# Kernel tuning notes

Measured on AMD Instinct MI355X. Metric: run time of the kernel, lower is better.

## Reference

```python
import jax, jax.numpy as jnp
import numpy as np

N, E = 50000, 800000
HID, HEADS, EDIM = 64, 4, 3
NEG_SLOPE = 0.2
LN_EPS = 1e-5


def setup_inputs() -> dict:
    key = jax.random.key(0)
    ks = jax.random.split(key, 12)
    h = jax.random.normal(ks[0], (N, HID), dtype=jnp.float32)
    edge_index = jax.random.randint(ks[1], (2, E), 0, N, dtype=jnp.int64)
    edge_attr = jax.random.normal(ks[2], (E, EDIM), dtype=jnp.float32)
    t = jax.random.uniform(ks[3], (1,), dtype=jnp.float32)
    s = 1.0 / np.sqrt(HID)
    W = jax.random.normal(ks[4], (HID, HEADS * HID), dtype=jnp.float32) * s
    att_src = jax.random.normal(ks[5], (1, HEADS, HID), dtype=jnp.float32) * s
    att_dst = jax.random.normal(ks[6], (1, HEADS, HID), dtype=jnp.float32) * s
    W_edge = jax.random.normal(ks[7], (EDIM, HEADS * HID), dtype=jnp.float32) * s
    att_edge = jax.random.normal(ks[8], (1, HEADS, HID), dtype=jnp.float32) * s
    bias = jnp.zeros((HID,), dtype=jnp.float32)
    ln_gamma = jnp.ones((HID,), dtype=jnp.float32)
    ln_beta = jnp.zeros((HID,), dtype=jnp.float32)
    return {"t": t, "h": h, "edge_index": edge_index, "edge_attr": edge_attr,
            "W": W, "att_src": att_src, "att_dst": att_dst, "W_edge": W_edge,
            "att_edge": att_edge, "bias": bias, "ln_gamma": ln_gamma, "ln_beta": ln_beta}


def reference(t, h, edge_index, edge_attr, W, att_src, att_dst, W_edge, att_edge, bias, ln_gamma, ln_beta):
    # GATConv (PyG, edge_dim>0, add_self_loops=False, concat=False, eval mode)
    x = (h @ W).reshape(N, HEADS, HID)                     # [N,H,C]
    a_src = (x * att_src).sum(-1)                          # [N,H]
    a_dst = (x * att_dst).sum(-1)                          # [N,H]
    e = (edge_attr @ W_edge).reshape(E, HEADS, HID)        # [E,H,C]
    a_edge = (e * att_edge).sum(-1)                        # [E,H]
    src, dst = edge_index[0], edge_index[1]
    alpha = a_src[src] + a_dst[dst] + a_edge               # [E,H]
    alpha = jax.nn.leaky_relu(alpha, NEG_SLOPE)
    # softmax over edges sharing the same destination node
    amax = jax.ops.segment_max(alpha, dst, num_segments=N)  # [N,H]
    ex = jnp.exp(alpha - amax[dst])
    esum = jax.ops.segment_sum(ex, dst, num_segments=N)     # [N,H]
    alpha = ex / (esum[dst] + 1e-16)
    msg = x[src] * alpha[:, :, None]                        # [E,H,C]
    out = jax.ops.segment_sum(msg, dst, num_segments=N)     # [N,H,C]
    out = out.mean(axis=1) + bias                           # concat=False -> head mean
    # LayerNorm + SiLU
    mu = out.mean(-1, keepdims=True)
    var = ((out - mu) ** 2).mean(-1, keepdims=True)
    y = (out - mu) * jax.lax.rsqrt(var + LN_EPS) * ln_gamma + ln_beta
    return y * jax.nn.sigmoid(y)
```

## Files before the change

kernel.cpp:

```cpp
#include <hip/hip_runtime.h>
#include <hip/hip_bf16.h>

#define HIDC 64
#define NEG_SLOPE 0.2f
#define SCAN_G 128

typedef __hip_bfloat16 bf16;
typedef short bf16x8 __attribute__((ext_vector_type(8)));
typedef float floatx4 __attribute__((ext_vector_type(4)));

static __device__ __forceinline__ float b2f(bf16 v) { return __bfloat162float(v); }

static __device__ __forceinline__ unsigned short f2us(float f) {
  bf16 b = __float2bfloat16(f);
  union { bf16 b; unsigned short u; } c;
  c.b = b;
  return c.u;
}

template <bool FF>
static __device__ __forceinline__ float ld(const void* __restrict__ p, size_t i) {
  return FF ? ((const float*)p)[i] : b2f(((const bf16*)p)[i]);
}
static __device__ __forceinline__ float ldr(const void* __restrict__ p, size_t i,
                                            bool ff) {
  return ff ? ((const float*)p)[i] : b2f(((const bf16*)p)[i]);
}
template <bool I64>
static __device__ __forceinline__ int ldi(const int* __restrict__ p, long long i) {
  return I64 ? (int)((const long long*)p)[i] : p[i];
}
static __device__ __forceinline__ int clampN(int v, int N) {
  return ((unsigned)v < (unsigned)N) ? v : 0;
}

static __device__ __forceinline__ bool det_f32(const unsigned* __restrict__ hw) {
  unsigned w = hw[threadIdx.x & 31];
  int ex = (w >> 7) & 0xFF;
  unsigned long long b = __ballot(ex >= 99 && ex <= 135);
  return __popcll(b) < 32;
}
static __device__ __forceinline__ bool det_i64(const int* __restrict__ ei) {
  int v = ei[2 * (threadIdx.x & 31) + 1];
  return __ballot(v != 0) == 0ULL;
}

template <bool FF, bool I64>
static __device__ __forceinline__ void xh_body(
    const void* __restrict__ h, const void* __restrict__ W,
    const void* __restrict__ att_src, const void* __restrict__ att_dst,
    const int* __restrict__ ei, bf16* __restrict__ x,
    float* __restrict__ a_src, float* __restrict__ a_dst,
    int* __restrict__ cnt, int N, int E,
    unsigned short* __restrict__ hls, unsigned short* __restrict__ wls) {
  for (long long e = (long long)blockIdx.x * 256 + threadIdx.x; e < E;
       e += (long long)gridDim.x * 256) {
    int dst = clampN(ldi<I64>(ei, (long long)E + e), N);
    atomicAdd(&cnt[dst], 1);
  }
  const int t = threadIdx.x;
  const long long n0 = (long long)blockIdx.x * 64;
  {
    const int c = t;
#pragma unroll
    for (int q = 0; q < 8; q++) {
      unsigned short u[8];
#pragma unroll
      for (int j = 0; j < 8; j++) {
        int k = q * 8 + j;
        u[j] = FF ? f2us(((const float*)W)[(size_t)k * 256 + c])
                  : ((const unsigned short*)W)[(size_t)k * 256 + c];
      }
      int4 v = make_int4((int)(u[0] | ((unsigned)u[1] << 16)),
                         (int)(u[2] | ((unsigned)u[3] << 16)),
                         (int)(u[4] | ((unsigned)u[5] << 16)),
                         (int)(u[6] | ((unsigned)u[7] << 16)));
      *(int4*)&wls[c * 64 + (q ^ (c & 7)) * 8] = v;
    }
  }
  {
    const int row = t >> 2;
    const long long n = n0 + row;
#pragma unroll
    for (int dq = 0; dq < 2; dq++) {
      int q = (t & 3) * 2 + dq;
      int4 v;
      if (n < N) {
        if (FF) {
          const float4* hp = (const float4*)h + n * 16 + q * 2;
          float4 f0 = hp[0], f1 = hp[1];
          v = make_int4((int)(f2us(f0.x) | ((unsigned)f2us(f0.y) << 16)),
                        (int)(f2us(f0.z) | ((unsigned)f2us(f0.w) << 16)),
                        (int)(f2us(f1.x) | ((unsigned)f2us(f1.y) << 16)),
                        (int)(f2us(f1.z) | ((unsigned)f2us(f1.w) << 16)));
        } else {
          v = *((const int4*)((const unsigned short*)h + n * 64 + q * 8));
        }
      } else {
        v = make_int4(0, 0, 0, 0);
      }
      *(int4*)&hls[row * 64 + (q ^ (row & 7)) * 8] = v;
    }
  }
  __syncthreads();
  const int w = t >> 6;
  const int lane = t & 63;
  const int lm = lane & 15, lq = lane >> 4;
  bf16x8 af[4][2];
#pragma unroll
  for (int nt = 0; nt < 4; nt++)
#pragma unroll
    for (int ks = 0; ks < 2; ks++) {
      int m = nt * 16 + lm;
      int q = ks * 4 + lq;
      af[nt][ks] = *(const bf16x8*)&hls[m * 64 + (q ^ (m & 7)) * 8];
    }
  floatx4 acc[4][4];
#pragma unroll
  for (int nt = 0; nt < 4; nt++)
#pragma unroll
    for (int ct = 0; ct < 4; ct++) acc[nt][ct] = (floatx4){0.f, 0.f, 0.f, 0.f};
#pragma unroll
  for (int ct = 0; ct < 4; ct++) {
    int c = w * 64 + ct * 16 + lm;
    bf16x8 b0 = *(const bf16x8*)&wls[c * 64 + ((lq) ^ (c & 7)) * 8];
    bf16x8 b1 = *(const bf16x8*)&wls[c * 64 + ((4 + lq) ^ (c & 7)) * 8];
#pragma unroll
    for (int nt = 0; nt < 4; nt++) {
      acc[nt][ct] = __builtin_amdgcn_mfma_f32_16x16x32_bf16(af[nt][0], b0,
                                                            acc[nt][ct], 0, 0, 0);
      acc[nt][ct] = __builtin_amdgcn_mfma_f32_16x16x32_bf16(af[nt][1], b1,
                                                            acc[nt][ct], 0, 0, 0);
    }
  }
  float as_c[4], ad_c[4];
#pragma unroll
  for (int ct = 0; ct < 4; ct++) {
    as_c[ct] = ld<FF>(att_src, w * 64 + ct * 16 + lm);
    ad_c[ct] = ld<FF>(att_dst, w * 64 + ct * 16 + lm);
  }
#pragma unroll
  for (int nt = 0; nt < 4; nt++) {
    float ps[4] = {0.f, 0.f, 0.f, 0.f}, pd[4] = {0.f, 0.f, 0.f, 0.f};
#pragma unroll
    for (int ct = 0; ct < 4; ct++) {
#pragma unroll
      for (int r = 0; r < 4; r++) {
        ps[r] += acc[nt][ct][r] * as_c[ct];
        pd[r] += acc[nt][ct][r] * ad_c[ct];
      }
    }
    long long nb = n0 + nt * 16 + lq * 4;
#pragma unroll
    for (int r = 0; r < 4; r++) {
      long long n = nb + r;
      if (n < N) {
#pragma unroll
        for (int ct = 0; ct < 4; ct++)
          x[n * 256 + w * 64 + ct * 16 + lm] = __float2bfloat16(acc[nt][ct][r]);
      }
    }
#pragma unroll
    for (int mask = 1; mask < 16; mask <<= 1) {
#pragma unroll
      for (int r = 0; r < 4; r++) {
        ps[r] += __shfl_xor(ps[r], mask);
        pd[r] += __shfl_xor(pd[r], mask);
      }
    }
    if (lm == 0) {
#pragma unroll
      for (int r = 0; r < 4; r++) {
        long long n = nb + r;
        if (n < N) {
          a_src[n * 4 + w] = ps[r];
          a_dst[n * 4 + w] = pd[r];
        }
      }
    }
  }
}

__global__ void __launch_bounds__(256) k_xh(
    const void* __restrict__ h, const void* __restrict__ W,
    const void* __restrict__ att_src, const void* __restrict__ att_dst,
    const int* __restrict__ ei, bf16* __restrict__ x,
    float* __restrict__ a_src, float* __restrict__ a_dst,
    int* __restrict__ cnt, int N, int E) {
  __shared__ alignas(16) unsigned short hls[64 * 64];
  __shared__ alignas(16) unsigned short wls[256 * 64];
  bool f32 = det_f32((const unsigned*)h);
  bool i64 = det_i64(ei);
  if (f32) {
    if (i64) xh_body<true, true>(h, W, att_src, att_dst, ei, x, a_src, a_dst, cnt, N, E, hls, wls);
    else     xh_body<true, false>(h, W, att_src, att_dst, ei, x, a_src, a_dst, cnt, N, E, hls, wls);
  } else {
    if (i64) xh_body<false, true>(h, W, att_src, att_dst, ei, x, a_src, a_dst, cnt, N, E, hls, wls);
    else     xh_body<false, false>(h, W, att_src, att_dst, ei, x, a_src, a_dst, cnt, N, E, hls, wls);
  }
}

__global__ void __launch_bounds__(1024) k_bscan(
    const void* __restrict__ W_edge, const void* __restrict__ att_edge,
    const unsigned* __restrict__ hw, const int* __restrict__ cnt,
    int* __restrict__ offs, int* __restrict__ bsum, int* __restrict__ bbase,
    int* __restrict__ done, float* __restrict__ M, int N) {
  int b = blockIdx.x, t = threadIdx.x;
  if (b == 0 && t < 768) {
    bool ff = det_f32(hw);
    int wv = t >> 6, lane = t & 63;
    int d = wv >> 2, hh = wv & 3;
    float p = ldr(W_edge, (size_t)d * 256 + hh * 64 + lane, ff) *
              ldr(att_edge, (size_t)hh * 64 + lane, ff);
#pragma unroll
    for (int o = 32; o; o >>= 1) p += __shfl_down(p, o);
    if (lane == 0) M[d * 4 + hh] = p;
  }
  const int C = (N + SCAN_G - 1) / SCAN_G;
  const int b0 = b * C;
  __shared__ int ts[1024];
  __shared__ int lastf;
  int v = 0;
  if (t < C && b0 + t < N) v = cnt[b0 + t];
  ts[t] = v;
  __syncthreads();
  for (int off = 1; off < 1024; off <<= 1) {
    int u = (t >= off) ? ts[t - off] : 0;
    __syncthreads();
    ts[t] += u;
    __syncthreads();
  }
  if (t < C && b0 + t < N) offs[b0 + t] = ts[t] - v;
  if (t == 1023) {
    atomicExch(&bsum[b], ts[1023]);
    __threadfence();
    int old = atomicAdd(done, 1);
    lastf = (old == SCAN_G - 1) ? 1 : 0;
  }
  __syncthreads();
  if (lastf) {
    int w = (t < SCAN_G) ? atomicAdd(&bsum[t], 0) : 0;
    ts[t] = w;
    __syncthreads();
    for (int off = 1; off < 1024; off <<= 1) {
      int u = (t >= off) ? ts[t - off] : 0;
      __syncthreads();
      ts[t] += u;
      __syncthreads();
    }
    if (t < SCAN_G) bbase[t] = ts[t] - w;
  }
}

__global__ void __launch_bounds__(1024) k_add(
    int* __restrict__ offs, int* __restrict__ cursor,
    const int* __restrict__ bbase, int N, int E) {
  int b = blockIdx.x, t = threadIdx.x;
  const int C = (N + SCAN_G - 1) / SCAN_G;
  const int b0 = b * C;
  int base = bbase[b];
  if (t < C && b0 + t < N) {
    int o = offs[b0 + t] + base;
    offs[b0 + t] = o;
    cursor[b0 + t] = o;
  }
  if (b == 0 && t == 0) offs[N] = E;
}

template <bool FF, bool I64>
static __device__ __forceinline__ void es_body(
    const int* __restrict__ ei, const void* __restrict__ eattr,
    const float* __restrict__ a_src, const float* __restrict__ a_dst,
    const float* __restrict__ M, int* __restrict__ cursor,
    int4* __restrict__ slots, int E, int N, unsigned* __restrict__ sattr) {
  const long long e0 = (long long)blockIdx.x * 256;
  {
    const unsigned bpe = FF ? 12u : 6u;
    const unsigned* gsrc = (const unsigned*)((const char*)eattr + e0 * bpe);
    unsigned ndw = FF ? 768u : 384u;
    long long bytes_left = ((long long)E - e0) * bpe;
    if (bytes_left < 0) bytes_left = 0;
    unsigned max_dw = (unsigned)((bytes_left + 3) >> 2);
    if (ndw > max_dw) ndw = max_dw;
    for (unsigned i = threadIdx.x; i < ndw; i += 256) sattr[i] = gsrc[i];
  }
  __syncthreads();
  long long e = e0 + threadIdx.x;
  if (e >= E) return;
  int src = clampN(ldi<I64>(ei, e), N);
  int dst = clampN(ldi<I64>(ei, (long long)E + e), N);
  float ea0, ea1, ea2;
  if (FF) {
    const float* sf = (const float*)sattr;
    ea0 = sf[threadIdx.x * 3 + 0];
    ea1 = sf[threadIdx.x * 3 + 1];
    ea2 = sf[threadIdx.x * 3 + 2];
  } else {
    const unsigned short* su = (const unsigned short*)sattr;
    ea0 = __uint_as_float((unsigned)su[threadIdx.x * 3 + 0] << 16);
    ea1 = __uint_as_float((unsigned)su[threadIdx.x * 3 + 1] << 16);
    ea2 = __uint_as_float((unsigned)su[threadIdx.x * 3 + 2] << 16);
  }
  const float4 m0 = ((const float4*)M)[0];
  const float4 m1 = ((const float4*)M)[1];
  const float4 m2 = ((const float4*)M)[2];
  const float4 as4 = ((const float4*)a_src)[src];
  const float4 ad4 = ((const float4*)a_dst)[dst];
  float al[4];
  al[0] = as4.x + ad4.x + ea0 * m0.x + ea1 * m1.x + ea2 * m2.x;
  al[1] = as4.y + ad4.y + ea0 * m0.y + ea1 * m1.y + ea2 * m2.y;
  al[2] = as4.z + ad4.z + ea0 * m0.z + ea1 * m1.z + ea2 * m2.z;
  al[3] = as4.w + ad4.w + ea0 * m0.w + ea1 * m1.w + ea2 * m2.w;
  unsigned short u[4];
#pragma unroll
  for (int hh = 0; hh < 4; hh++) {
    float a = al[hh];
    a = (a > 0.f) ? a : NEG_SLOPE * a;
    a = fminf(fmaxf(a, -60.f), 60.f);
    u[hh] = f2us(__expf(a));
  }
  int pos = atomicAdd(&cursor[dst], 1);
  slots[pos] = make_int4(src, (int)(u[0] | ((unsigned)u[1] << 16)),
                         (int)(u[2] | ((unsigned)u[3] << 16)), 0);
}

__global__ void __launch_bounds__(256) k_es(
    const int* __restrict__ ei, const void* __restrict__ eattr,
    const float* __restrict__ a_src, const float* __restrict__ a_dst,
    const float* __restrict__ M, const unsigned* __restrict__ hw,
    int* __restrict__ cursor, int4* __restrict__ slots, int E, int N) {
  __shared__ unsigned sattr[768];
  bool f32 = det_f32(hw);
  bool i64 = det_i64(ei);
  if (f32) {
    if (i64) es_body<true, true>(ei, eattr, a_src, a_dst, M, cursor, slots, E, N, sattr);
    else     es_body<true, false>(ei, eattr, a_src, a_dst, M, cursor, slots, E, N, sattr);
  } else {
    if (i64) es_body<false, true>(ei, eattr, a_src, a_dst, M, cursor, slots, E, N, sattr);
    else     es_body<false, false>(ei, eattr, a_src, a_dst, M, cursor, slots, E, N, sattr);
  }
}

template <bool HZ>
static __device__ __forceinline__ void agg_loop(
    const int4* __restrict__ slots, const unsigned* __restrict__ xw,
    int s0, int s1, bool hi_half, float& a0o, float& a1o, float& wso) {
  float a0 = 0.f, a1 = 0.f, ws = 0.f;
  int i = s0;
  for (; i + 4 <= s1; i += 4) {
    int4 q0 = slots[i], q1 = slots[i + 1], q2 = slots[i + 2], q3 = slots[i + 3];
    unsigned d0 = xw[(size_t)((unsigned)q0.x << 7)];
    unsigned d1 = xw[(size_t)((unsigned)q1.x << 7)];
    unsigned d2 = xw[(size_t)((unsigned)q2.x << 7)];
    unsigned d3 = xw[(size_t)((unsigned)q3.x << 7)];
    unsigned p0 = HZ ? (unsigned)q0.z : (unsigned)q0.y;
    unsigned p1 = HZ ? (unsigned)q1.z : (unsigned)q1.y;
    unsigned p2 = HZ ? (unsigned)q2.z : (unsigned)q2.y;
    unsigned p3 = HZ ? (unsigned)q3.z : (unsigned)q3.y;
    float w0 = __uint_as_float(hi_half ? (p0 & 0xffff0000u) : (p0 << 16));
    float w1 = __uint_as_float(hi_half ? (p1 & 0xffff0000u) : (p1 << 16));
    float w2 = __uint_as_float(hi_half ? (p2 & 0xffff0000u) : (p2 << 16));
    float w3 = __uint_as_float(hi_half ? (p3 & 0xffff0000u) : (p3 << 16));
    a0 += w0 * __uint_as_float(d0 << 16);
    a1 += w0 * __uint_as_float(d0 & 0xffff0000u);
    a0 += w1 * __uint_as_float(d1 << 16);
    a1 += w1 * __uint_as_float(d1 & 0xffff0000u);
    a0 += w2 * __uint_as_float(d2 << 16);
    a1 += w2 * __uint_as_float(d2 & 0xffff0000u);
    a0 += w3 * __uint_as_float(d3 << 16);
    a1 += w3 * __uint_as_float(d3 & 0xffff0000u);
    ws += (w0 + w1) + (w2 + w3);
  }
  for (; i < s1; i++) {
    int4 q = slots[i];
    unsigned d = xw[(size_t)((unsigned)q.x << 7)];
    unsigned pz = HZ ? (unsigned)q.z : (unsigned)q.y;
    float wv = __uint_as_float(hi_half ? (pz & 0xffff0000u) : (pz << 16));
    a0 += wv * __uint_as_float(d << 16);
    a1 += wv * __uint_as_float(d & 0xffff0000u);
    ws += wv;
  }
  a0o = a0; a1o = a1; wso = ws;
}

__global__ void __launch_bounds__(256) k_agg(
    const int* __restrict__ offs, const int4* __restrict__ slots,
    const unsigned* __restrict__ xu, const unsigned* __restrict__ hw,
    const void* __restrict__ bias, const void* __restrict__ gamma,
    const void* __restrict__ beta, void* __restrict__ out, int N) {
  __shared__ float sh[2][256];
  int t = threadIdx.x;
  int w = t >> 6, lane = t & 63;
  int nl = w >> 1;
  int hb2 = w & 1;
  int n = blockIdx.x * 2 + nl;
  if (n < N) {
    const unsigned* xw = xu + hb2 * 64 + lane;
    int s0 = offs[n], s1 = offs[n + 1];
    bool hi_half = lane >= 32;
    float a0, a1, ws;
    if (hb2) agg_loop<true>(slots, xw, s0, s1, hi_half, a0, a1, ws);
    else     agg_loop<false>(slots, xw, s0, s1, hi_half, a0, a1, ws);
    float inv = 1.f / (ws + 1e-16f);
    int head = hb2 * 2 + (hi_half ? 1 : 0);
    int pidx = lane & 31;
    sh[nl][head * 64 + 2 * pidx] = a0 * inv;
    sh[nl][head * 64 + 2 * pidx + 1] = a1 * inv;
  }
  __syncthreads();
  if ((t & 127) < 64) {
    int nl2 = t >> 7;
    int n2 = blockIdx.x * 2 + nl2;
    if (n2 < N) {
      int c = t & 63;
      bool ff = det_f32(hw);
      float m = (sh[nl2][c] + sh[nl2][64 + c] + sh[nl2][128 + c] +
                 sh[nl2][192 + c]) * 0.25f + ldr(bias, c, ff);
      float mu = m;
#pragma unroll
      for (int off = 32; off; off >>= 1) mu += __shfl_xor(mu, off);
      mu *= (1.f / 64.f);
      float d = m - mu;
      float v = d * d;
#pragma unroll
      for (int off = 32; off; off >>= 1) v += __shfl_xor(v, off);
      v *= (1.f / 64.f);
      float y = d * rsqrtf(v + 1e-5f) * ldr(gamma, c, ff) + ldr(beta, c, ff);
      float sig = 1.f / (1.f + __expf(-y));
      float r = y * sig;
      size_t oi = (size_t)n2 * 64 + c;
      if (ff) ((float*)out)[oi] = r;
      else ((bf16*)out)[oi] = __float2bfloat16(r);
    }
  }
}

extern "C" void kernel_launch(void* const* d_in, const int* in_sizes, int n_in,
                              void* d_out, int out_size, void* d_ws,
                              size_t ws_size, hipStream_t stream) {
  const void* h        = d_in[1];
  const int*  ei       = (const int*)d_in[2];
  const void* eattr    = d_in[3];
  const void* W        = d_in[4];
  const void* att_src  = d_in[5];
  const void* att_dst  = d_in[6];
  const void* W_edge   = d_in[7];
  const void* att_edge = d_in[8];
  const void* bias     = d_in[9];
  const void* gamma    = d_in[10];
  const void* beta     = d_in[11];

  const int N = in_sizes[1] / HIDC;
  const int E = in_sizes[3] / 3;

  char* p = (char*)d_ws;
  float* M    = (float*)p; p += 64;
  bf16* x     = (bf16*)p;  p += (size_t)N * 256 * 2;
  float* asrc = (float*)p; p += (size_t)N * 4 * 4;
  float* adst = (float*)p; p += (size_t)N * 4 * 4;
  int4* slots = (int4*)p;  p += (size_t)E * 16;
  int* cnt    = (int*)p;   p += (size_t)N * 4;
  int* done   = (int*)p;   p += 64;
  int* offs   = (int*)p;   p += ((size_t)N + 4) * 4;
  int* cursor = (int*)p;   p += (size_t)N * 4;
  int* bsum   = (int*)p;   p += SCAN_G * 4;
  int* bbase  = (int*)p;   p += SCAN_G * 4;

  size_t need = (size_t)(p - (char*)d_ws);
  if (ws_size < need || N <= 0 || E <= 0) {
    hipMemsetAsync(d_out, 0, (size_t)out_size * 2, stream);
    return;
  }

  hipMemsetAsync(cnt, 0, (size_t)N * 4 + 64, stream);

  k_xh<<<(N + 63) / 64, 256, 0, stream>>>(h, W, att_src, att_dst, ei, x,
                                          asrc, adst, cnt, N, E);
  k_bscan<<<SCAN_G, 1024, 0, stream>>>(W_edge, att_edge, (const unsigned*)h,
                                       cnt, offs, bsum, bbase, done, M, N);
  k_add<<<SCAN_G, 1024, 0, stream>>>(offs, cursor, bbase, N, E);
  k_es<<<(E + 255) / 256, 256, 0, stream>>>(ei, eattr, asrc, adst, M,
                                            (const unsigned*)h, cursor, slots,
                                            E, N);
  k_agg<<<(N + 1) / 2, 256, 0, stream>>>(offs, slots, (const unsigned*)x,
                                         (const unsigned*)h, bias, gamma, beta,
                                         d_out, N);
}
```

Measured before the change: 279.4 us.

## Aggregate one node per wavefront with 8-byte gathers and shuffle-based LayerNorm

The aggregation kernel now gives each wavefront a whole destination node instead of splitting a node across two wavefronts. Each lane gathers a uint2, four bf16 values, per source edge, so one wave reads the full 256-element row. Head reduction and LayerNorm statistics are done with cross-lane shuffles instead of shared memory and a block barrier. Source indices and offsets are made wave-uniform with readfirstlane. This halves the slot reads per node and removes the __syncthreads, at the cost of more accumulators per lane and only a quarter of the lanes doing the final writes.

```diff
diff --git a/kernel.cpp b/kernel.cpp
--- a/kernel.cpp
+++ b/kernel.cpp
@@ -341,46 +341,10 @@
   }
 }
 
-template <bool HZ>
-static __device__ __forceinline__ void agg_loop(
-    const int4* __restrict__ slots, const unsigned* __restrict__ xw,
-    int s0, int s1, bool hi_half, float& a0o, float& a1o, float& wso) {
-  float a0 = 0.f, a1 = 0.f, ws = 0.f;
-  int i = s0;
-  for (; i + 4 <= s1; i += 4) {
-    int4 q0 = slots[i], q1 = slots[i + 1], q2 = slots[i + 2], q3 = slots[i + 3];
-    unsigned d0 = xw[(size_t)((unsigned)q0.x << 7)];
-    unsigned d1 = xw[(size_t)((unsigned)q1.x << 7)];
-    unsigned d2 = xw[(size_t)((unsigned)q2.x << 7)];
-    unsigned d3 = xw[(size_t)((unsigned)q3.x << 7)];
-    unsigned p0 = HZ ? (unsigned)q0.z : (unsigned)q0.y;
-    unsigned p1 = HZ ? (unsigned)q1.z : (unsigned)q1.y;
-    unsigned p2 = HZ ? (unsigned)q2.z : (unsigned)q2.y;
-    unsigned p3 = HZ ? (unsigned)q3.z : (unsigned)q3.y;
-    float w0 = __uint_as_float(hi_half ? (p0 & 0xffff0000u) : (p0 << 16));
-    float w1 = __uint_as_float(hi_half ? (p1 & 0xffff0000u) : (p1 << 16));
-    float w2 = __uint_as_float(hi_half ? (p2 & 0xffff0000u) : (p2 << 16));
-    float w3 = __uint_as_float(hi_half ? (p3 & 0xffff0000u) : (p3 << 16));
-    a0 += w0 * __uint_as_float(d0 << 16);
-    a1 += w0 * __uint_as_float(d0 & 0xffff0000u);
-    a0 += w1 * __uint_as_float(d1 << 16);
-    a1 += w1 * __uint_as_float(d1 & 0xffff0000u);
-    a0 += w2 * __uint_as_float(d2 << 16);
-    a1 += w2 * __uint_as_float(d2 & 0xffff0000u);
-    a0 += w3 * __uint_as_float(d3 << 16);
-    a1 += w3 * __uint_as_float(d3 & 0xffff0000u);
-    ws += (w0 + w1) + (w2 + w3);
-  }
-  for (; i < s1; i++) {
-    int4 q = slots[i];
-    unsigned d = xw[(size_t)((unsigned)q.x << 7)];
-    unsigned pz = HZ ? (unsigned)q.z : (unsigned)q.y;
-    float wv = __uint_as_float(hi_half ? (pz & 0xffff0000u) : (pz << 16));
-    a0 += wv * __uint_as_float(d << 16);
-    a1 += wv * __uint_as_float(d & 0xffff0000u);
-    ws += wv;
-  }
-  a0o = a0; a1o = a1; wso = ws;
+static __device__ __forceinline__ uint2 xgat(const uint2* __restrict__ xr,
+                                             int src, int lane) {
+  int ss = __builtin_amdgcn_readfirstlane(src);
+  return xr[(size_t)(unsigned)ss * 64 + lane];
 }
 
 __global__ void __launch_bounds__(256) k_agg(
@@ -388,49 +352,102 @@
     const unsigned* __restrict__ xu, const unsigned* __restrict__ hw,
     const void* __restrict__ bias, const void* __restrict__ gamma,
     const void* __restrict__ beta, void* __restrict__ out, int N) {
-  __shared__ float sh[2][256];
-  int t = threadIdx.x;
-  int w = t >> 6, lane = t & 63;
-  int nl = w >> 1;
-  int hb2 = w & 1;
-  int n = blockIdx.x * 2 + nl;
-  if (n < N) {
-    const unsigned* xw = xu + hb2 * 64 + lane;
-    int s0 = offs[n], s1 = offs[n + 1];
-    bool hi_half = lane >= 32;
-    float a0, a1, ws;
-    if (hb2) agg_loop<true>(slots, xw, s0, s1, hi_half, a0, a1, ws);
-    else     agg_loop<false>(slots, xw, s0, s1, hi_half, a0, a1, ws);
-    float inv = 1.f / (ws + 1e-16f);
-    int head = hb2 * 2 + (hi_half ? 1 : 0);
-    int pidx = lane & 31;
-    sh[nl][head * 64 + 2 * pidx] = a0 * inv;
-    sh[nl][head * 64 + 2 * pidx + 1] = a1 * inv;
-  }
-  __syncthreads();
-  if ((t & 127) < 64) {
-    int nl2 = t >> 7;
-    int n2 = blockIdx.x * 2 + nl2;
-    if (n2 < N) {
-      int c = t & 63;
-      bool ff = det_f32(hw);
-      float m = (sh[nl2][c] + sh[nl2][64 + c] + sh[nl2][128 + c] +
-                 sh[nl2][192 + c]) * 0.25f + ldr(bias, c, ff);
-      float mu = m;
-#pragma unroll
-      for (int off = 32; off; off >>= 1) mu += __shfl_xor(mu, off);
-      mu *= (1.f / 64.f);
-      float d = m - mu;
-      float v = d * d;
-#pragma unroll
-      for (int off = 32; off; off >>= 1) v += __shfl_xor(v, off);
-      v *= (1.f / 64.f);
-      float y = d * rsqrtf(v + 1e-5f) * ldr(gamma, c, ff) + ldr(beta, c, ff);
-      float sig = 1.f / (1.f + __expf(-y));
-      float r = y * sig;
-      size_t oi = (size_t)n2 * 64 + c;
-      if (ff) ((float*)out)[oi] = r;
-      else ((bf16*)out)[oi] = __float2bfloat16(r);
+  const int t = threadIdx.x;
+  const int wv = t >> 6, lane = t & 63;
+  const int n = blockIdx.x * 4 + wv;
+  if (n >= N) return;
+  const int head2 = lane >> 5;
+  const unsigned wshift = (lane & 16) ? 0u : 16u;
+  const uint2* __restrict__ xr = (const uint2*)xu;
+
+  int s0 = __builtin_amdgcn_readfirstlane(offs[n]);
+  int s1 = __builtin_amdgcn_readfirstlane(offs[n + 1]);
+
+  float a0 = 0.f, a1 = 0.f, a2 = 0.f, a3 = 0.f, ws = 0.f;
+  int i = s0;
+  for (; i + 4 <= s1; i += 4) {
+    int4 q0 = slots[i], q1 = slots[i + 1], q2 = slots[i + 2], q3 = slots[i + 3];
+    uint2 d0 = xgat(xr, q0.x, lane);
+    uint2 d1 = xgat(xr, q1.x, lane);
+    uint2 d2 = xgat(xr, q2.x, lane);
+    uint2 d3 = xgat(xr, q3.x, lane);
+    unsigned e0 = head2 ? (unsigned)q0.z : (unsigned)q0.y;
+    unsigned e1 = head2 ? (unsigned)q1.z : (unsigned)q1.y;
+    unsigned e2 = head2 ? (unsigned)q2.z : (unsigned)q2.y;
+    unsigned e3 = head2 ? (unsigned)q3.z : (unsigned)q3.y;
+    float w0 = __uint_as_float((e0 << wshift) & 0xffff0000u);
+    float w1 = __uint_as_float((e1 << wshift) & 0xffff0000u);
+    float w2 = __uint_as_float((e2 << wshift) & 0xffff0000u);
+    float w3 = __uint_as_float((e3 << wshift) & 0xffff0000u);
+    a0 += w0 * __uint_as_float(d0.x << 16);
+    a1 += w0 * __uint_as_float(d0.x & 0xffff0000u);
+    a2 += w0 * __uint_as_float(d0.y << 16);
+    a3 += w0 * __uint_as_float(d0.y & 0xffff0000u);
+    a0 += w1 * __uint_as_float(d1.x << 16);
+    a1 += w1 * __uint_as_float(d1.x & 0xffff0000u);
+    a2 += w1 * __uint_as_float(d1.y << 16);
+    a3 += w1 * __uint_as_float(d1.y & 0xffff0000u);
+    a0 += w2 * __uint_as_float(d2.x << 16);
+    a1 += w2 * __uint_as_float(d2.x & 0xffff0000u);
+    a2 += w2 * __uint_as_float(d2.y << 16);
+    a3 += w2 * __uint_as_float(d2.y & 0xffff0000u);
+    a0 += w3 * __uint_as_float(d3.x << 16);
+    a1 += w3 * __uint_as_float(d3.x & 0xffff0000u);
+    a2 += w3 * __uint_as_float(d3.y << 16);
+    a3 += w3 * __uint_as_float(d3.y & 0xffff0000u);
+    ws += (w0 + w1) + (w2 + w3);
+  }
+  for (; i < s1; i++) {
+    int4 q = slots[i];
+    uint2 d = xgat(xr, q.x, lane);
+    unsigned e = head2 ? (unsigned)q.z : (unsigned)q.y;
+    float w = __uint_as_float((e << wshift) & 0xffff0000u);
+    a0 += w * __uint_as_float(d.x << 16);
+    a1 += w * __uint_as_float(d.x & 0xffff0000u);
+    a2 += w * __uint_as_float(d.y << 16);
+    a3 += w * __uint_as_float(d.y & 0xffff0000u);
+    ws += w;
+  }
+
+  float inv = 1.f / (ws + 1e-16f);
+  float v0 = a0 * inv, v1 = a1 * inv, v2 = a2 * inv, v3 = a3 * inv;
+  v0 += __shfl_xor(v0, 16); v1 += __shfl_xor(v1, 16);
+  v2 += __shfl_xor(v2, 16); v3 += __shfl_xor(v3, 16);
+  v0 += __shfl_xor(v0, 32); v1 += __shfl_xor(v1, 32);
+  v2 += __shfl_xor(v2, 32); v3 += __shfl_xor(v3, 32);
+
+  bool ff = det_f32(hw);
+  const int c0 = (lane & 15) * 4;
+  float m0 = v0 * 0.25f + ldr(bias, c0 + 0, ff);
+  float m1 = v1 * 0.25f + ldr(bias, c0 + 1, ff);
+  float m2 = v2 * 0.25f + ldr(bias, c0 + 2, ff);
+  float m3 = v3 * 0.25f + ldr(bias, c0 + 3, ff);
+
+  float s = (m0 + m1) + (m2 + m3);
+  s += __shfl_xor(s, 1); s += __shfl_xor(s, 2);
+  s += __shfl_xor(s, 4); s += __shfl_xor(s, 8);
+  float mu = s * 0.015625f;
+  float d0 = m0 - mu, d1 = m1 - mu, d2 = m2 - mu, d3 = m3 - mu;
+  float vq = (d0 * d0 + d1 * d1) + (d2 * d2 + d3 * d3);
+  vq += __shfl_xor(vq, 1); vq += __shfl_xor(vq, 2);
+  vq += __shfl_xor(vq, 4); vq += __shfl_xor(vq, 8);
+  float rstd = rsqrtf(vq * 0.015625f + 1e-5f);
+
+  if ((lane >> 4) == 0) {
+    float y0 = d0 * rstd * ldr(gamma, c0 + 0, ff) + ldr(beta, c0 + 0, ff);
+    float y1 = d1 * rstd * ldr(gamma, c0 + 1, ff) + ldr(beta, c0 + 1, ff);
+    float y2 = d2 * rstd * ldr(gamma, c0 + 2, ff) + ldr(beta, c0 + 2, ff);
+    float y3 = d3 * rstd * ldr(gamma, c0 + 3, ff) + ldr(beta, c0 + 3, ff);
+    float r0 = y0 / (1.f + __expf(-y0));
+    float r1 = y1 / (1.f + __expf(-y1));
+    float r2 = y2 / (1.f + __expf(-y2));
+    float r3 = y3 / (1.f + __expf(-y3));
+    size_t ob = (size_t)n * 64 + c0;
+    if (ff) {
+      *(float4*)((float*)out + ob) = make_float4(r0, r1, r2, r3);
+    } else {
+      *(ushort4*)((bf16*)out + ob) =
+          make_ushort4(f2us(r0), f2us(r1), f2us(r2), f2us(r3));
     }
   }
 }
@@ -482,7 +499,7 @@
   k_es<<<(E + 255) / 256, 256, 0, stream>>>(ei, eattr, asrc, adst, M,
                                             (const unsigned*)h, cursor, slots,
                                             E, N);
-  k_agg<<<(N + 1) / 2, 256, 0, stream>>>(offs, slots, (const unsigned*)x,
+  k_agg<<<(N + 3) / 4, 256, 0, stream>>>(offs, slots, (const unsigned*)x,
                                          (const unsigned*)h, bias, gamma, beta,
                                          d_out, N);
 }
```

New measurement: 266.8 us. 4.5% less time.
